# Kernel optimization log

Hardware: AMD Instinct MI355X
Metric: run time of the kernel (lower is better)

Reference implementation:

```python
import jax, jax.numpy as jnp
import numpy as np

DIM = 384
HEADS = 12
HEAD_DIM = DIM // HEADS
WS = 7          # window_size
SS = 3          # shift_size (SW-MSA)
DIM_FF = 4 * DIM
EPS = 1e-5


def _rel_pos_index():
    coords = np.stack(np.meshgrid(np.arange(WS), np.arange(WS), indexing='ij'))
    cf = coords.reshape(2, -1)                       # (2, 49)
    rel = cf[:, :, None] - cf[:, None, :]            # (2, 49, 49)
    rel = rel.transpose(1, 2, 0).astype(np.int64)
    rel[:, :, 0] += WS - 1
    rel[:, :, 1] += WS - 1
    rel[:, :, 0] *= 2 * WS - 1
    return rel.sum(-1)                               # (49, 49)


def _attn_mask(Hp, Wp):
    # cyclic-shift mask, computed on static shapes with numpy
    img = np.zeros((Hp, Wp))
    slices = (slice(0, -WS), slice(-WS, -SS), slice(-SS, None))
    cnt = 0
    for hs in slices:
        for ws_ in slices:
            img[hs, ws_] = cnt
            cnt += 1
    mw = img.reshape(Hp // WS, WS, Wp // WS, WS).transpose(0, 2, 1, 3).reshape(-1, WS * WS)
    am = mw[:, None, :] - mw[:, :, None]             # unsqueeze(1) - unsqueeze(2)
    am = np.where(am != 0, -100.0, 0.0)
    return jnp.asarray(am, jnp.float32)              # (nW, 49, 49)


def _ln(x, g, b):
    mu = jnp.mean(x, -1, keepdims=True)
    var = jnp.mean(jnp.square(x - mu), -1, keepdims=True)
    return (x - mu) * jax.lax.rsqrt(var + EPS) * g + b


def setup_inputs() -> dict:
    key = jax.random.key(0)
    ks = jax.random.split(key, 8)
    B, H, W = 32, 56, 56
    s = 0.02
    return {
        'x': jax.random.normal(ks[0], (B, H * W, DIM), jnp.float32),
        'H': H, 'W': W,
        'rel_idx': jnp.asarray(_rel_pos_index(), jnp.int32),
        'rpb_table': jax.random.normal(ks[1], ((2 * WS - 1) ** 2, HEADS), jnp.float32) * s,
        'qkv_w': jax.random.normal(ks[2], (DIM, 3 * DIM), jnp.float32) * s,
        'proj_w': jax.random.normal(ks[3], (DIM, DIM), jnp.float32) * s,
        'proj_b': jnp.zeros((DIM,), jnp.float32),
        'norm1_g': jnp.ones((DIM,), jnp.float32),
        'norm1_b': jnp.zeros((DIM,), jnp.float32),
        'norm2_g': jnp.ones((DIM,), jnp.float32),
        'norm2_b': jnp.zeros((DIM,), jnp.float32),
        'ffn_w1': jax.random.normal(ks[4], (DIM, DIM_FF), jnp.float32) * s,
        'ffn_b1': jnp.zeros((DIM_FF,), jnp.float32),
        'ffn_w2': jax.random.normal(ks[5], (DIM_FF, DIM), jnp.float32) * s,
        'ffn_b2': jnp.zeros((DIM,), jnp.float32),
    }


def reference(x, H, W, rel_idx, rpb_table, qkv_w, proj_w, proj_b,
              norm1_g, norm1_b, norm2_g, norm2_b,
              ffn_w1, ffn_b1, ffn_w2, ffn_b2):
    B, L, C = x.shape
    shortcut = x
    h = _ln(x, norm1_g, norm1_b).reshape(B, H, W, C)

    pad_b = (WS - H % WS) % WS
    pad_r = (WS - W % WS) % WS
    if pad_b > 0 or pad_r > 0:
        h = jnp.pad(h, ((0, 0), (0, pad_b), (0, pad_r), (0, 0)))
    Hp, Wp = H + pad_b, W + pad_r

    if SS > 0:
        h = jnp.roll(h, (-SS, -SS), axis=(1, 2))

    # window partition -> (B*nW, 49, C)
    nHw, nWw = Hp // WS, Wp // WS
    win = h.reshape(B, nHw, WS, nWw, WS, C).transpose(0, 1, 3, 2, 4, 5)
    win = win.reshape(-1, WS * WS, C)
    Bw, N = win.shape[0], WS * WS

    # window attention
    qkv = (win @ qkv_w).reshape(Bw, N, 3, HEADS, HEAD_DIM)
    q, k, v = [qkv[:, :, i].transpose(0, 2, 1, 3) for i in range(3)]  # (Bw, heads, N, hd)
    attn = jnp.einsum('bhnd,bhmd->bhnm', q, k) / np.sqrt(HEAD_DIM)

    bias = rpb_table[rel_idx]                      # (N, N, heads)
    attn = attn + bias.transpose(2, 0, 1)[None]

    if SS > 0:
        mask = _attn_mask(Hp, Wp)                  # (nW, N, N)
        nW = mask.shape[0]
        attn = attn.reshape(B, nW, HEADS, N, N) + mask[None, :, None]
        attn = attn.reshape(Bw, HEADS, N, N)

    attn = jax.nn.softmax(attn, axis=-1)
    out = jnp.einsum('bhnm,bhmd->bnhd', attn, v).reshape(Bw, N, C)
    out = out @ proj_w + proj_b

    # window reverse
    out = out.reshape(B, nHw, nWw, WS, WS, C).transpose(0, 1, 3, 2, 4, 5)
    out = out.reshape(B, Hp, Wp, C)
    if SS > 0:
        out = jnp.roll(out, (SS, SS), axis=(1, 2))
    if pad_b > 0 or pad_r > 0:
        out = out[:, :H, :W, :]

    h = shortcut + out.reshape(B, H * W, C)
    ff = _ln(h, norm2_g, norm2_b)
    ff = jax.nn.gelu(ff @ ffn_w1 + ffn_b1, approximate=False) @ ffn_w2 + ffn_b2
    return h + ff
```

## Files before the change

kernel.cpp:

```cpp
#include <hip/hip_runtime.h>

#define DEV __device__ __forceinline__

typedef __bf16 bf16x8 __attribute__((ext_vector_type(8)));
typedef float  f32x4  __attribute__((ext_vector_type(4)));
typedef unsigned short u16x8 __attribute__((ext_vector_type(8)));
typedef unsigned short u16x4 __attribute__((ext_vector_type(4)));
typedef long  longx2 __attribute__((ext_vector_type(2)));

DEV float b2f(unsigned short u) {
    unsigned int t = ((unsigned int)u) << 16;
    return __uint_as_float(t);
}
DEV unsigned short f2b(float f) {
    unsigned int u = __float_as_uint(f);
    unsigned int r = (u + 0x7FFFu + ((u >> 16) & 1u)) >> 16;
    return (unsigned short)r;
}
DEV unsigned char f2f8(float f) {
    return (unsigned char)(__builtin_amdgcn_cvt_pk_fp8_f32(f, f, 0, false) & 0xff);
}

DEV int kpos(int c) {
    int s = (c >> 3) & 7;
    return (c & ~63) | ((((s & 3) << 1) | (s >> 2)) << 3) | (c & 7);
}

DEV void gload_lds16(const void* g, void* l) {
    __builtin_amdgcn_global_load_lds(
        (const __attribute__((address_space(1))) void*)g,
        (__attribute__((address_space(3))) void*)l, 16, 0, 0);
}

DEV size_t win_to_tok(int row) {
    int w = row / 49, t = row - w * 49;
    int b  = w >> 6, widx = w & 63;
    int wi = widx >> 3, wj = widx & 7;
    int ti = t / 7, tj = t - ti * 7;
    int hh = wi * 7 + ti + 3; if (hh >= 56) hh -= 56;
    int ww = wj * 7 + tj + 3; if (ww >= 56) ww -= 56;
    return (size_t)b * 3136 + (size_t)hh * 56 + ww;
}

__global__ void tokmap_build(int* __restrict__ tm, int T) {
    int i = blockIdx.x * 256 + threadIdx.x;
    if (i < T) tm[i] = (int)win_to_tok(i);
}

__global__ void wprep8(const float* __restrict__ src, unsigned char* __restrict__ dst,
                       int K, int N) {
    int idx = blockIdx.x * 256 + threadIdx.x;
    if (idx >= K * N) return;
    int k = idx / N, n = idx - k * N;
    dst[(size_t)n * K + kpos(k)] = f2f8(src[idx]);
}

__global__ void btab_build(const int* __restrict__ rel_idx, const float* __restrict__ rpb,
                           float* __restrict__ tab) {
    int idx = blockIdx.x * 256 + threadIdx.x;
    if (idx >= 4 * 12 * 64 * 64) return;
    int col = idx & 63, row = (idx >> 6) & 63;
    int h = (idx >> 12) % 12, cls = idx / (12 * 4096);
    float v;
    if (row >= 49 || col >= 49) {
        v = -10000.f;
    } else {
        v = rpb[rel_idx[row * 49 + col] * 12 + h];
        int ti = row / 7, tj = row - (row / 7) * 7;
        int si = col / 7, sj = col - (col / 7) * 7;
        int lq = ((cls & 2) ? (ti < 4 ? 1 : 2) : 0) * 3 + ((cls & 1) ? (tj < 4 ? 1 : 2) : 0);
        int lk = ((cls & 2) ? (si < 4 ? 1 : 2) : 0) * 3 + ((cls & 1) ? (sj < 4 ? 1 : 2) : 0);
        if (lq != lk) v -= 100.f;
    }
    tab[idx] = v;
}

template <int REMAP>
__global__ __launch_bounds__(256) void ln_kernel(const float* __restrict__ x,
                                                 const float* __restrict__ g,
                                                 const float* __restrict__ b,
                                                 unsigned char* __restrict__ out,
                                                 int rows) {
    int r = blockIdx.x * 4 + (threadIdx.x >> 6);
    int lane = threadIdx.x & 63;
    if (r >= rows) return;
    size_t src = REMAP ? win_to_tok(r) : (size_t)r;
    const float* xp = x + src * 384;
    float v[6];
    float s = 0.f;
#pragma unroll
    for (int i = 0; i < 6; ++i) { v[i] = xp[i * 64 + lane]; s += v[i]; }
#pragma unroll
    for (int off = 32; off; off >>= 1) s += __shfl_xor(s, off, 64);
    float mu = s * (1.f / 384.f);
    float q = 0.f;
#pragma unroll
    for (int i = 0; i < 6; ++i) { float d = v[i] - mu; q += d * d; }
#pragma unroll
    for (int off = 32; off; off >>= 1) q += __shfl_xor(q, off, 64);
    float inv = rsqrtf(q * (1.f / 384.f) + 1e-5f);
    unsigned char* op = out + (size_t)r * 384;
#pragma unroll
    for (int i = 0; i < 6; ++i) {
        int c = i * 64 + lane;
        op[kpos(c)] = f2f8((v[i] - mu) * inv * g[c] + b[c]);
    }
}

template <int MODE>
__global__ __launch_bounds__(256, 2) void gemm_f8_fullk(const unsigned char* __restrict__ A,
                                                        const unsigned char* __restrict__ Bt,
                                                        int M, int N, int K,
                                                        const float* __restrict__ bias,
                                                        const float* __restrict__ resid,
                                                        const int* __restrict__ tokmap,
                                                        unsigned char* __restrict__ outb8,
                                                        float* __restrict__ outf) {
    __shared__ unsigned char Als[64 * 384];
    __shared__ unsigned char Bls[128 * 384];
    const int tid = threadIdx.x;
    const int wid = tid >> 6, lane = tid & 63;
    const int ntile = N >> 7;

    int bid = blockIdx.x;
    int nwg = gridDim.x;
    int swb = ((nwg & 7) == 0) ? ((bid & 7) * (nwg >> 3) + (bid >> 3)) : bid;
    const int mt = swb / ntile, nt = swb - mt * ntile;

    const unsigned char* Abase = A  + (size_t)(mt * 64) * K;
    const unsigned char* Bbase = Bt + (size_t)(nt * 128) * K;

    {
        int rA = tid >> 2;
        int gpA = (tid & 3) ^ ((rA >> 1) & 3);
#pragma unroll
        for (int kb = 0; kb < 6; ++kb)
            gload_lds16(Abase + (size_t)rA * K + kb * 64 + gpA * 16, &Als[kb * 4096 + tid * 16]);
#pragma unroll
        for (int kb = 0; kb < 6; ++kb)
#pragma unroll
            for (int j = 0; j < 2; ++j) {
                int r = j * 64 + (tid >> 2);
                int gp = (tid & 3) ^ ((r >> 1) & 3);
                gload_lds16(Bbase + (size_t)r * K + kb * 64 + gp * 16,
                            &Bls[kb * 8192 + j * 4096 + tid * 16]);
            }
    }
    asm volatile("s_waitcnt vmcnt(0)" ::: "memory");
    __builtin_amdgcn_s_barrier();

    const int fr = lane & 15, kq = lane >> 4;
    const int cb = (kq ^ ((fr >> 1) & 3)) << 4;

    f32x4 acc[4][2] = {};
#pragma unroll
    for (int kb = 0; kb < 6; ++kb) {
        longx2 a[4], b[2];
#pragma unroll
        for (int m = 0; m < 4; ++m)
            a[m] = *(const longx2*)(&Als[kb * 4096 + (m * 16 + fr) * 64 + cb]);
#pragma unroll
        for (int n = 0; n < 2; ++n)
            b[n] = *(const longx2*)(&Bls[kb * 8192 + (wid * 32 + n * 16 + fr) * 64 + cb]);
#pragma unroll
        for (int ks = 0; ks < 2; ++ks)
#pragma unroll
            for (int m = 0; m < 4; ++m)
#pragma unroll
                for (int n = 0; n < 2; ++n)
                    acc[m][n] = __builtin_amdgcn_mfma_f32_16x16x32_fp8_fp8(b[n][ks], a[m][ks], acc[m][n], 0, 0, 0);
    }

    const int row0 = mt * 64;
    const int col0 = nt * 128 + wid * 32;
    const int rl = lane & 15;
    const int cq = (lane >> 4) << 2;
#pragma unroll
    for (int m = 0; m < 4; ++m) {
        int row = row0 + m * 16 + rl;
        size_t tok = 0;
        if constexpr (MODE == 1) tok = (size_t)tokmap[row];
#pragma unroll
        for (int n = 0; n < 2; ++n) {
            int col = col0 + n * 16 + cq;
            f32x4 v = acc[m][n];
            if constexpr (MODE == 0) {
                int pk = 0;
                pk = __builtin_amdgcn_cvt_pk_fp8_f32(v[0], v[1], pk, false);
                pk = __builtin_amdgcn_cvt_pk_fp8_f32(v[2], v[3], pk, true);
                *(int*)(outb8 + (size_t)row * N + col) = pk;
            } else if constexpr (MODE == 1) {
                size_t o = tok * 384 + col;
                f32x4 rv = *(const f32x4*)&resid[o];
                f32x4 bb = *(const f32x4*)&bias[col];
                f32x4 ov = rv + v + bb;
                *(f32x4*)&outf[o] = ov;
            } else {
                f32x4 bb = *(const f32x4*)&bias[col];
                float g4[4];
#pragma unroll
                for (int r = 0; r < 4; ++r) {
                    float t2 = v[r] + bb[r];
                    float e  = __expf(-1.702f * t2);
                    g4[r] = t2 * __builtin_amdgcn_rcpf(1.f + e);
                }
                int pk = 0;
                pk = __builtin_amdgcn_cvt_pk_fp8_f32(g4[0], g4[1], pk, false);
                pk = __builtin_amdgcn_cvt_pk_fp8_f32(g4[2], g4[3], pk, true);
                *(int*)(outb8 + (size_t)row * N + kpos(col)) = pk;
            }
        }
    }
}

template <int NBUF, int DEPTH, int MINW>
__global__ __launch_bounds__(256, MINW) void gemm_f8_ring(const unsigned char* __restrict__ A,
                                                          const unsigned char* __restrict__ Bt,
                                                          int M, int N, int K,
                                                          const float* __restrict__ bias,
                                                          const float* __restrict__ resid,
                                                          float* __restrict__ outf) {
    static_assert(NBUF >= DEPTH + 2, "ring too small");
    __shared__ unsigned char As[NBUF][128 * 64];
    __shared__ unsigned char Bs[NBUF][128 * 64];
    const int tid = threadIdx.x;
    const int wid = tid >> 6, lane = tid & 63;
    const int ntile = N >> 7;

    int bid = blockIdx.x;
    int nwg = gridDim.x;
    int swb = ((nwg & 7) == 0) ? ((bid & 7) * (nwg >> 3) + (bid >> 3)) : bid;
    const int mt = swb / ntile, nt = swb - mt * ntile;
    const int wr = wid >> 1, wc = wid & 1;

    f32x4 acc[4][4] = {};

    const unsigned char* Abase = A  + (size_t)(mt * 128) * K;
    const unsigned char* Bbase = Bt + (size_t)(nt * 128) * K;

    auto stage = [&](int buf, int k0) {
#pragma unroll
        for (int j = 0; j < 2; ++j) {
            int r  = j * 64 + (tid >> 2);
            int gp = (tid & 3) ^ ((r >> 1) & 3);
            gload_lds16(Abase + (size_t)r * K + k0 + gp * 16, &As[buf][j * 4096 + tid * 16]);
            gload_lds16(Bbase + (size_t)r * K + k0 + gp * 16, &Bs[buf][j * 4096 + tid * 16]);
        }
    };

    const int fr = lane & 15, kq = lane >> 4;
    const int rowA = wr * 64 + fr;
    const int rowB = wc * 64 + fr;
    const int cb = (kq ^ ((fr >> 1) & 3)) << 4;

    const int nk = K >> 6;
    stage(0, 0);
    if (nk > 1) stage(1, 64);

    for (int t = 0; t < nk; ++t) {
        const int cur = t % NBUF;
        if (t + DEPTH < nk) {
            stage((t + DEPTH) % NBUF, (t + DEPTH) << 6);
            asm volatile("s_waitcnt vmcnt(8)" ::: "memory");
        } else if (t + 1 < nk) {
            asm volatile("s_waitcnt vmcnt(4)" ::: "memory");
        } else {
            asm volatile("s_waitcnt vmcnt(0)" ::: "memory");
        }
        __builtin_amdgcn_s_barrier();

        longx2 a[4], b[4];
#pragma unroll
        for (int m = 0; m < 4; ++m)
            a[m] = *(const longx2*)(&As[cur][(rowA + m * 16) * 64 + cb]);
#pragma unroll
        for (int n = 0; n < 4; ++n)
            b[n] = *(const longx2*)(&Bs[cur][(rowB + n * 16) * 64 + cb]);
#pragma unroll
        for (int ks = 0; ks < 2; ++ks)
#pragma unroll
            for (int m = 0; m < 4; ++m)
#pragma unroll
                for (int n = 0; n < 4; ++n)
                    acc[m][n] = __builtin_amdgcn_mfma_f32_16x16x32_fp8_fp8(b[n][ks], a[m][ks], acc[m][n], 0, 0, 0);

        asm volatile("s_waitcnt lgkmcnt(0)" ::: "memory");
    }

    const int row0 = mt * 128 + wr * 64;
    const int col0 = nt * 128 + wc * 64;
    const int rl = lane & 15;
    const int cq = (lane >> 4) << 2;
#pragma unroll
    for (int m = 0; m < 4; ++m) {
        int row = row0 + m * 16 + rl;
#pragma unroll
        for (int n = 0; n < 4; ++n) {
            int col = col0 + n * 16 + cq;
            f32x4 v = acc[m][n];
            size_t o = (size_t)row * N + col;
            f32x4 rv = *(const f32x4*)&resid[o];
            f32x4 bb = *(const f32x4*)&bias[col];
            f32x4 ov = rv + v + bb;
            *(f32x4*)&outf[o] = ov;
        }
    }
}

__global__ __launch_bounds__(256, 2) void attn_kernel(const unsigned char* __restrict__ QKV8,
                                                      const float* __restrict__ Btab,
                                                      unsigned char* __restrict__ O8) {
    __shared__ char lds[8192 + 16384 + 32768];
    char* Kl = lds;
    char* Vl = lds + 8192;
    char* Pl = lds + 24576;

    const int w   = blockIdx.x;
    const int tid = threadIdx.x, wid = tid >> 6, lane = tid & 63;
    const int fr  = lane & 15, kq = lane >> 4;
    const size_t base = (size_t)w * 49 * 1152;
    const int widx = w & 63, wi = widx >> 3, wj = widx & 7;
    const int cls = ((wi == 7) ? 2 : 0) | ((wj == 7) ? 1 : 0);
    const float* tb = Btab + (size_t)cls * 12 * 4096;
    constexpr float SCL = 0.17677669529663687f;

    for (int R = 0; R < 3; ++R) {
        if (R) __syncthreads();
        {
            f32x4 z = {};
#pragma unroll
            for (int j = 0; j < 6; ++j) *(f32x4*)(lds + j * 4096 + tid * 16) = z;
        }
        __syncthreads();
        {
            int hh = tid >> 6, h = R * 4 + hh;
#pragma unroll
            for (int it = 0; it < 4; ++it) {
                int i = (tid & 63) + it * 64;
                if (i < 196) {
                    int m = i >> 2, c = i & 3;
                    long k8 = *(const long*)(QKV8 + base + (size_t)m * 1152 + 384 + h * 32 + c * 8);
                    int s = c ^ (m & 3) ^ ((m >> 2) & 3);
                    *(long*)(Kl + hh * 2048 + m * 32 + s * 8) = k8;
                    long v8 = *(const long*)(QKV8 + base + (size_t)m * 1152 + 768 + h * 32 + c * 8);
                    int lo = (int)v8, hi = (int)(v8 >> 32);
                    float vf[8];
                    vf[0] = __builtin_amdgcn_cvt_f32_fp8(lo, 0);
                    vf[1] = __builtin_amdgcn_cvt_f32_fp8(lo, 1);
                    vf[2] = __builtin_amdgcn_cvt_f32_fp8(lo, 2);
                    vf[3] = __builtin_amdgcn_cvt_f32_fp8(lo, 3);
                    vf[4] = __builtin_amdgcn_cvt_f32_fp8(hi, 0);
                    vf[5] = __builtin_amdgcn_cvt_f32_fp8(hi, 1);
                    vf[6] = __builtin_amdgcn_cvt_f32_fp8(hi, 2);
                    vf[7] = __builtin_amdgcn_cvt_f32_fp8(hi, 3);
#pragma unroll
                    for (int j = 0; j < 8; ++j) {
                        int d = c * 8 + j;
                        *(unsigned short*)(Vl + hh * 4096 + d * 128 +
                                           (((m >> 3) ^ (d & 7)) * 16) + (m & 7) * 2) = f2b(vf[j]);
                    }
                }
            }
        }
        __syncthreads();

        const int h = R * 4 + wid;
        const float* tbh = tb + h * 4096;

        long aq[4], bk[4];
#pragma unroll
        for (int mi = 0; mi < 4; ++mi) {
            int row = mi * 16 + fr; if (row > 48) row = 48;
            aq[mi] = *(const long*)(QKV8 + base + (size_t)row * 1152 + h * 32 + kq * 8);
        }
#pragma unroll
        for (int ni = 0; ni < 4; ++ni) {
            int rk = ni * 16 + fr;
            bk[ni] = *(const long*)(Kl + wid * 2048 + rk * 32 +
                                    ((kq ^ (rk & 3) ^ ((rk >> 2) & 3)) * 8));
        }
        f32x4 s[4][4] = {};
#pragma unroll
        for (int mi = 0; mi < 4; ++mi)
#pragma unroll
            for (int ni = 0; ni < 4; ++ni)
                s[mi][ni] = __builtin_amdgcn_mfma_f32_16x16x32_fp8_fp8(bk[ni], aq[mi], s[mi][ni], 0, 0, 0);

        float linv_[4];
#pragma unroll
        for (int mi = 0; mi < 4; ++mi) {
            int row = mi * 16 + fr;
            const float* tr = tbh + row * 64 + kq * 4;
            f32x4 sv[4];
            float mx = -1e30f;
#pragma unroll
            for (int ni = 0; ni < 4; ++ni) {
                f32x4 bb = *(const f32x4*)&tr[ni * 16];
                sv[ni] = s[mi][ni] * SCL + bb;
                mx = fmaxf(mx, fmaxf(fmaxf(sv[ni][0], sv[ni][1]), fmaxf(sv[ni][2], sv[ni][3])));
            }
            mx = fmaxf(mx, __shfl_xor(mx, 16, 64));
            mx = fmaxf(mx, __shfl_xor(mx, 32, 64));
            float sm = 0.f;
#pragma unroll
            for (int ni = 0; ni < 4; ++ni)
#pragma unroll
                for (int r = 0; r < 4; ++r) { sv[ni][r] = __expf(sv[ni][r] - mx); sm += sv[ni][r]; }
            sm += __shfl_xor(sm, 16, 64);
            sm += __shfl_xor(sm, 32, 64);
            linv_[mi] = __builtin_amdgcn_rcpf(sm);
#pragma unroll
            for (int ni = 0; ni < 4; ++ni) {
                int colb = ni * 16 + kq * 4;
                int phys = (colb >> 3) ^ (row & 7);
                u16x4 pk;
#pragma unroll
                for (int r = 0; r < 4; ++r) pk[r] = f2b(sv[ni][r]);
                *(u16x4*)(Pl + wid * 8192 + row * 128 + phys * 16 + (colb & 7) * 2) = pk;
            }
        }
        asm volatile("s_waitcnt lgkmcnt(0)" ::: "memory");
        __builtin_amdgcn_sched_barrier(0);

        f32x4 oacc[4][2] = {};
#pragma unroll
        for (int sl = 0; sl < 2; ++sl) {
            bf16x8 bv[2];
#pragma unroll
            for (int ni = 0; ni < 2; ++ni) {
                int d = ni * 16 + fr;
                bv[ni] = *(const bf16x8*)(Vl + wid * 4096 + d * 128 + (((sl * 4 + kq) ^ (d & 7)) * 16));
            }
#pragma unroll
            for (int mi = 0; mi < 4; ++mi) {
                int row = mi * 16 + fr;
                bf16x8 ap = *(const bf16x8*)(Pl + wid * 8192 + row * 128 + (((sl * 4 + kq) ^ (row & 7)) * 16));
#pragma unroll
                for (int ni = 0; ni < 2; ++ni)
                    oacc[mi][ni] = __builtin_amdgcn_mfma_f32_16x16x32_bf16(bv[ni], ap, oacc[mi][ni], 0, 0, 0);
            }
        }

#pragma unroll
        for (int mi = 0; mi < 4; ++mi) {
            int row = mi * 16 + fr;
            if (row < 49) {
                float li = linv_[mi];
                unsigned char* opb = O8 + (size_t)(w * 49 + row) * 384;
#pragma unroll
                for (int ni = 0; ni < 2; ++ni) {
                    int c = h * 32 + ni * 16 + kq * 4;
                    int pk = 0;
                    pk = __builtin_amdgcn_cvt_pk_fp8_f32(oacc[mi][ni][0] * li, oacc[mi][ni][1] * li, pk, false);
                    pk = __builtin_amdgcn_cvt_pk_fp8_f32(oacc[mi][ni][2] * li, oacc[mi][ni][3] * li, pk, true);
                    *(int*)(opb + kpos(c)) = pk;
                }
            }
        }
    }
}

extern "C" void kernel_launch(void* const* d_in, const int* in_sizes, int n_in,
                              void* d_out, int out_size, void* d_ws, size_t ws_size,
                              hipStream_t stream) {
    const float* x     = (const float*)d_in[0];
    const int*   rel   = (const int*)  d_in[3];
    const float* rpb   = (const float*)d_in[4];
    const float* qkvw  = (const float*)d_in[5];
    const float* projw = (const float*)d_in[6];
    const float* projb = (const float*)d_in[7];
    const float* n1g   = (const float*)d_in[8];
    const float* n1b   = (const float*)d_in[9];
    const float* n2g   = (const float*)d_in[10];
    const float* n2b   = (const float*)d_in[11];
    const float* w1    = (const float*)d_in[12];
    const float* b1    = (const float*)d_in[13];
    const float* w2    = (const float*)d_in[14];
    const float* b2    = (const float*)d_in[15];
    float* out = (float*)d_out;

    const int T = in_sizes[0] / 384;

    char* ws = (char*)d_ws;
    size_t off = 0;
    auto alloc = [&](size_t bytes) {
        char* p = ws + off;
        off += (bytes + 255) & ~(size_t)255;
        return p;
    };
    unsigned char* Wq8  = (unsigned char*)alloc((size_t)1152 * 384);
    unsigned char* Wp8  = (unsigned char*)alloc((size_t)384 * 384);
    unsigned char* W18  = (unsigned char*)alloc((size_t)1536 * 384);
    unsigned char* W28  = (unsigned char*)alloc((size_t)384 * 1536);
    float*         Btab = (float*)       alloc((size_t)4 * 12 * 4096 * 4);
    int*           Tmap = (int*)         alloc((size_t)T * 4);
    unsigned char* slotA = (unsigned char*)alloc((size_t)T * 384);
    unsigned char* slotB = (unsigned char*)alloc((size_t)T * 1536);

    unsigned char* X1   = slotA;
    unsigned char* O8   = slotA;
    unsigned char* X2   = slotA;
    unsigned char* QKV8 = slotB;
    unsigned char* F8   = slotB;
    float*         Hh   = out;

    wprep8<<<dim3((1152 * 384 + 255) / 256), 256, 0, stream>>>(qkvw, Wq8, 384, 1152);
    wprep8<<<dim3((384 * 384 + 255) / 256),  256, 0, stream>>>(projw, Wp8, 384, 384);
    wprep8<<<dim3((384 * 1536 + 255) / 256), 256, 0, stream>>>(w1, W18, 384, 1536);
    wprep8<<<dim3((1536 * 384 + 255) / 256), 256, 0, stream>>>(w2, W28, 1536, 384);
    btab_build<<<dim3((4 * 12 * 4096 + 255) / 256), 256, 0, stream>>>(rel, rpb, Btab);
    tokmap_build<<<dim3((T + 255) / 256), 256, 0, stream>>>(Tmap, T);

    ln_kernel<1><<<dim3(T / 4), 256, 0, stream>>>(x, n1g, n1b, X1, T);
    gemm_f8_fullk<0><<<dim3((T / 64) * (1152 / 128)), 256, 0, stream>>>(
        X1, Wq8, T, 1152, 384, nullptr, nullptr, nullptr, QKV8, nullptr);
    attn_kernel<<<dim3(T / 49), 256, 0, stream>>>(QKV8, Btab, O8);
    gemm_f8_fullk<1><<<dim3((T / 64) * (384 / 128)), 256, 0, stream>>>(
        O8, Wp8, T, 384, 384, projb, x, Tmap, nullptr, Hh);
    ln_kernel<0><<<dim3(T / 4), 256, 0, stream>>>(Hh, n2g, n2b, X2, T);
    gemm_f8_fullk<2><<<dim3((T / 64) * (1536 / 128)), 256, 0, stream>>>(
        X2, W18, T, 1536, 384, b1, nullptr, nullptr, F8, nullptr);
    gemm_f8_ring<4, 2, 2><<<dim3((T / 128) * (384 / 128)), 256, 0, stream>>>(
        F8, W28, T, 384, 1536, b2, Hh, out);
}
```

Measured before the change: 656.4 us.

## Use 8 waves per block in full-K fp8 GEMM, each wave owning 16 columns

The full-K fp8 GEMM now launches 512 threads (8 waves) per block instead of 256. Each wave computes a 64x16 output slice rather than 64x32, so per-wave accumulators and B-fragment loads are halved. The LDS staging is redistributed: all threads load B and the first 256 load A. The aim is more waves per CU to hide LDS and MFMA latency, at the cost of more redundant A-fragment LDS reads per block and a heavier block footprint.

New measurement: 636.1 us. 1.03x faster.

```diff
diff --git a/kernel.cpp b/kernel.cpp
--- a/kernel.cpp
+++ b/kernel.cpp
@@ -108,7 +108,7 @@
 }
 
 template <int MODE>
-__global__ __launch_bounds__(256, 2) void gemm_f8_fullk(const unsigned char* __restrict__ A,
+__global__ __launch_bounds__(512, 2) void gemm_f8_fullk(const unsigned char* __restrict__ A,
                                                         const unsigned char* __restrict__ Bt,
                                                         int M, int N, int K,
                                                         const float* __restrict__ bias,
@@ -131,20 +131,18 @@
     const unsigned char* Bbase = Bt + (size_t)(nt * 128) * K;
 
     {
-        int rA = tid >> 2;
-        int gpA = (tid & 3) ^ ((rA >> 1) & 3);
+        int rB = tid >> 2;
+        int gpB = (tid & 3) ^ ((rB >> 1) & 3);
 #pragma unroll
         for (int kb = 0; kb < 6; ++kb)
-            gload_lds16(Abase + (size_t)rA * K + kb * 64 + gpA * 16, &Als[kb * 4096 + tid * 16]);
-#pragma unroll
-        for (int kb = 0; kb < 6; ++kb)
-#pragma unroll
-            for (int j = 0; j < 2; ++j) {
-                int r = j * 64 + (tid >> 2);
-                int gp = (tid & 3) ^ ((r >> 1) & 3);
-                gload_lds16(Bbase + (size_t)r * K + kb * 64 + gp * 16,
-                            &Bls[kb * 8192 + j * 4096 + tid * 16]);
-            }
+            gload_lds16(Bbase + (size_t)rB * K + kb * 64 + gpB * 16, &Bls[kb * 8192 + tid * 16]);
+        if (tid < 256) {
+            int rA = tid >> 2;
+            int gpA = (tid & 3) ^ ((rA >> 1) & 3);
+#pragma unroll
+            for (int kb = 0; kb < 6; ++kb)
+                gload_lds16(Abase + (size_t)rA * K + kb * 64 + gpA * 16, &Als[kb * 4096 + tid * 16]);
+        }
     }
     asm volatile("s_waitcnt vmcnt(0)" ::: "memory");
     __builtin_amdgcn_s_barrier();
@@ -152,63 +150,54 @@
     const int fr = lane & 15, kq = lane >> 4;
     const int cb = (kq ^ ((fr >> 1) & 3)) << 4;
 
-    f32x4 acc[4][2] = {};
+    f32x4 acc[4] = {};
 #pragma unroll
     for (int kb = 0; kb < 6; ++kb) {
-        longx2 a[4], b[2];
+        longx2 a[4], b;
+        b = *(const longx2*)(&Bls[kb * 8192 + (wid * 16 + fr) * 64 + cb]);
 #pragma unroll
         for (int m = 0; m < 4; ++m)
             a[m] = *(const longx2*)(&Als[kb * 4096 + (m * 16 + fr) * 64 + cb]);
 #pragma unroll
-        for (int n = 0; n < 2; ++n)
-            b[n] = *(const longx2*)(&Bls[kb * 8192 + (wid * 32 + n * 16 + fr) * 64 + cb]);
-#pragma unroll
         for (int ks = 0; ks < 2; ++ks)
 #pragma unroll
             for (int m = 0; m < 4; ++m)
-#pragma unroll
-                for (int n = 0; n < 2; ++n)
-                    acc[m][n] = __builtin_amdgcn_mfma_f32_16x16x32_fp8_fp8(b[n][ks], a[m][ks], acc[m][n], 0, 0, 0);
+                acc[m] = __builtin_amdgcn_mfma_f32_16x16x32_fp8_fp8(b[ks], a[m][ks], acc[m], 0, 0, 0);
     }
 
     const int row0 = mt * 64;
-    const int col0 = nt * 128 + wid * 32;
+    const int col0 = nt * 128 + wid * 16;
     const int rl = lane & 15;
     const int cq = (lane >> 4) << 2;
+    const int col = col0 + cq;
 #pragma unroll
     for (int m = 0; m < 4; ++m) {
         int row = row0 + m * 16 + rl;
-        size_t tok = 0;
-        if constexpr (MODE == 1) tok = (size_t)tokmap[row];
-#pragma unroll
-        for (int n = 0; n < 2; ++n) {
-            int col = col0 + n * 16 + cq;
-            f32x4 v = acc[m][n];
-            if constexpr (MODE == 0) {
-                int pk = 0;
-                pk = __builtin_amdgcn_cvt_pk_fp8_f32(v[0], v[1], pk, false);
-                pk = __builtin_amdgcn_cvt_pk_fp8_f32(v[2], v[3], pk, true);
-                *(int*)(outb8 + (size_t)row * N + col) = pk;
-            } else if constexpr (MODE == 1) {
-                size_t o = tok * 384 + col;
-                f32x4 rv = *(const f32x4*)&resid[o];
-                f32x4 bb = *(const f32x4*)&bias[col];
-                f32x4 ov = rv + v + bb;
-                *(f32x4*)&outf[o] = ov;
-            } else {
-                f32x4 bb = *(const f32x4*)&bias[col];
-                float g4[4];
-#pragma unroll
-                for (int r = 0; r < 4; ++r) {
-                    float t2 = v[r] + bb[r];
-                    float e  = __expf(-1.702f * t2);
-                    g4[r] = t2 * __builtin_amdgcn_rcpf(1.f + e);
-                }
-                int pk = 0;
-                pk = __builtin_amdgcn_cvt_pk_fp8_f32(g4[0], g4[1], pk, false);
-                pk = __builtin_amdgcn_cvt_pk_fp8_f32(g4[2], g4[3], pk, true);
-                *(int*)(outb8 + (size_t)row * N + kpos(col)) = pk;
-            }
+        f32x4 v = acc[m];
+        if constexpr (MODE == 0) {
+            int pk = 0;
+            pk = __builtin_amdgcn_cvt_pk_fp8_f32(v[0], v[1], pk, false);
+            pk = __builtin_amdgcn_cvt_pk_fp8_f32(v[2], v[3], pk, true);
+            *(int*)(outb8 + (size_t)row * N + col) = pk;
+        } else if constexpr (MODE == 1) {
+            size_t o = (size_t)tokmap[row] * 384 + col;
+            f32x4 rv = *(const f32x4*)&resid[o];
+            f32x4 bb = *(const f32x4*)&bias[col];
+            f32x4 ov = rv + v + bb;
+            *(f32x4*)&outf[o] = ov;
+        } else {
+            f32x4 bb = *(const f32x4*)&bias[col];
+            float g4[4];
+#pragma unroll
+            for (int r = 0; r < 4; ++r) {
+                float t2 = v[r] + bb[r];
+                float e  = __expf(-1.702f * t2);
+                g4[r] = t2 * __builtin_amdgcn_rcpf(1.f + e);
+            }
+            int pk = 0;
+            pk = __builtin_amdgcn_cvt_pk_fp8_f32(g4[0], g4[1], pk, false);
+            pk = __builtin_amdgcn_cvt_pk_fp8_f32(g4[2], g4[3], pk, true);
+            *(int*)(outb8 + (size_t)row * N + kpos(col)) = pk;
         }
     }
 }
@@ -512,13 +501,13 @@
     tokmap_build<<<dim3((T + 255) / 256), 256, 0, stream>>>(Tmap, T);
 
     ln_kernel<1><<<dim3(T / 4), 256, 0, stream>>>(x, n1g, n1b, X1, T);
-    gemm_f8_fullk<0><<<dim3((T / 64) * (1152 / 128)), 256, 0, stream>>>(
+    gemm_f8_fullk<0><<<dim3((T / 64) * (1152 / 128)), 512, 0, stream>>>(
         X1, Wq8, T, 1152, 384, nullptr, nullptr, nullptr, QKV8, nullptr);
     attn_kernel<<<dim3(T / 49), 256, 0, stream>>>(QKV8, Btab, O8);
-    gemm_f8_fullk<1><<<dim3((T / 64) * (384 / 128)), 256, 0, stream>>>(
+    gemm_f8_fullk<1><<<dim3((T / 64) * (384 / 128)), 512, 0, stream>>>(
         O8, Wp8, T, 384, 384, projb, x, Tmap, nullptr, Hh);
     ln_kernel<0><<<dim3(T / 4), 256, 0, stream>>>(Hh, n2g, n2b, X2, T);
-    gemm_f8_fullk<2><<<dim3((T / 64) * (1536 / 128)), 256, 0, stream>>>(
+    gemm_f8_fullk<2><<<dim3((T / 64) * (1536 / 128)), 512, 0, stream>>>(
         X2, W18, T, 1536, 384, b1, nullptr, nullptr, F8, nullptr);
     gemm_f8_ring<4, 2, 2><<<dim3((T / 128) * (384 / 128)), 256, 0, stream>>>(
         F8, W28, T, 384, 1536, b2, Hh, out);
```
